# Kernel optimization log

Hardware: AMD Instinct MI355X
Metric: run time of the kernel (lower is better)

## Reference

```python
import jax, jax.numpy as jnp
import numpy as np
from jax import lax

MAP = 64  # spatial map resolution, hard-coded in the module


def setup_inputs() -> dict:
    key = jax.random.key(0)
    ks = jax.random.split(key, 6)
    B, N = 8, 17
    # valid boxes [x0,y0,x1,y1] inside the 64x64 map
    mins = jax.random.uniform(ks[0], (B, N, 2), jnp.float32) * 40.0
    sizes = jax.random.uniform(ks[1], (B, N, 2), jnp.float32) * 20.0 + 4.0
    bboxes = jnp.concatenate([mins, mins + sizes], axis=-1)  # [B,N,4]
    conv1_w = jax.random.normal(ks[2], (64, 2, 5, 5), jnp.float32) * 0.1
    conv1_b = jnp.zeros((64,), jnp.float32)
    conv2_w = jax.random.normal(ks[3], (32, 64, 5, 5), jnp.float32) * 0.05
    conv2_b = jnp.zeros((32,), jnp.float32)
    fc_w = jax.random.normal(ks[4], (512, 32), jnp.float32) * 0.1
    fc_b = jnp.zeros((512,), jnp.float32)
    return dict(bboxes=bboxes, conv1_w=conv1_w, conv1_b=conv1_b,
                conv2_w=conv2_w, conv2_b=conv2_b, fc_w=fc_w, fc_b=fc_b)


def _build_sp_maps(bboxes):
    # bboxes: [B,N,4] -> pairwise 2-channel binary maps [P, 2, 64, 64]
    B, N, _ = bboxes.shape
    iu, ju = jnp.triu_indices(N, k=1)           # P0 = N*(N-1)/2 pairs
    box_i = bboxes[:, iu]                       # [B,P0,4]
    box_j = bboxes[:, ju]                       # [B,P0,4]
    boxes = jnp.stack([box_i, box_j], axis=2)   # [B,P0,2,4]
    boxes = boxes.reshape(-1, 2, 4)             # [P,2,4]
    ys = jnp.arange(MAP, dtype=jnp.float32)[:, None]   # [64,1]
    xs = jnp.arange(MAP, dtype=jnp.float32)[None, :]   # [1,64]
    x0 = boxes[..., 0][..., None, None]
    y0 = boxes[..., 1][..., None, None]
    x1 = boxes[..., 2][..., None, None]
    y1 = boxes[..., 3][..., None, None]
    inside = (xs >= x0) & (xs < x1) & (ys >= y0) & (ys < y1)
    sp = inside.astype(bboxes.dtype)            # [P,2,64,64]
    # slicing tensor (batch, i, j) per pair
    P0 = iu.shape[0]
    b_idx = jnp.repeat(jnp.arange(B), P0)
    slicing = jnp.stack([b_idx, jnp.tile(iu, B), jnp.tile(ju, B)], axis=1)
    return sp, slicing


def _conv(x, w, b):
    y = lax.conv_general_dilated(x, w, (1, 1), 'VALID',
                                 dimension_numbers=('NCHW', 'OIHW', 'NCHW'))
    return y + b[None, :, None, None]


def _maxpool2(x):
    return lax.reduce_window(x, -jnp.inf, lax.max, (1, 1, 2, 2), (1, 1, 2, 2), 'VALID')


def reference(bboxes, conv1_w, conv1_b, conv2_w, conv2_b, fc_w, fc_b):
    sp, slicing = _build_sp_maps(bboxes)        # [P,2,64,64]
    h = _maxpool2(_conv(sp, conv1_w, conv1_b))  # [P,64,30,30]
    h = _maxpool2(_conv(h, conv2_w, conv2_b))   # [P,32,13,13]
    h = jnp.mean(h, axis=(2, 3))                # AvgPool(13) -> [P,32]
    feat = jax.nn.relu(h @ fc_w.T + fc_b)       # [P,512]
    return feat, slicing
```

## Files before the change

kernel.cpp:

```cpp
#include <hip/hip_runtime.h>
#include <hip/hip_bf16.h>


#define NPAIRS 1088
#define FEAT_SZ (NPAIRS * 512)

typedef float f32x16 __attribute__((ext_vector_type(16)));
typedef int v8i __attribute__((ext_vector_type(8)));
typedef float floatx2 __attribute__((ext_vector_type(2)));

#define WS_V 0
#define WS_C2B 14400
#define WS_BFRAG 14528

#define H1_PLANE 7200
#define H1_BYTES 57600
#define SM_V 57600
#define SM_HM 72000
#define SM_PART 72128
#define SMEM_BYTES 74176

__device__ __forceinline__ unsigned short f2bf(float f) {
  __hip_bfloat16 h = __float2bfloat16(f);
  unsigned short u;
  __builtin_memcpy(&u, &h, 2);
  return u;
}
__device__ __forceinline__ float bflo(unsigned int u) { return __uint_as_float(u << 16); }
__device__ __forceinline__ float bfhi(unsigned int u) { return __uint_as_float(u & 0xffff0000u); }

__device__ __forceinline__ void fp8x8_to_f32(uint2 u, float* f) {
  floatx2 t;
  t = __builtin_amdgcn_cvt_pk_f32_fp8((int)u.x, false); f[0] = t.x; f[1] = t.y;
  t = __builtin_amdgcn_cvt_pk_f32_fp8((int)u.x, true);  f[2] = t.x; f[3] = t.y;
  t = __builtin_amdgcn_cvt_pk_f32_fp8((int)u.y, false); f[4] = t.x; f[5] = t.y;
  t = __builtin_amdgcn_cvt_pk_f32_fp8((int)u.y, true);  f[6] = t.x; f[7] = t.y;
}

__device__ __forceinline__ void pair_ij(int k, int* pi, int* pj) {
  int i = 0, rem = k;
  while (rem >= 16 - i) { rem -= 16 - i; ++i; }
  *pi = i;
  *pj = i + 1 + rem;
}

__device__ __forceinline__ int stz(int z, int a, int b) {
  if (z >= a) {
    if (z >= b) return 0;
    if (z <= b - 5) return 5;
    return 5 + (b - z);
  }
  if (z >= a - 4) return a - z;
  return 0;
}

__global__ void prep_kernel(const float* __restrict__ w1, const float* __restrict__ b1,
                            const float* __restrict__ w2, float* __restrict__ out,
                            unsigned char* __restrict__ ws) {
  int tid = blockIdx.x * blockDim.x + threadIdx.x;

  if (tid < 12800) {
    int o = tid & 63;
    int q = tid >> 6;
    int sx = q % 10; q /= 10;
    int sy = q % 10;
    int c = q / 10;
    int ky0 = (sy <= 4) ? sy : 0;
    int ky1 = (sy == 0) ? 0 : ((sy <= 5) ? 5 : sy - 5);
    int kx0 = (sx <= 4) ? sx : 0;
    int kx1 = (sx == 0) ? 0 : ((sx <= 5) ? 5 : sx - 5);
    const float* w = w1 + (o * 2 + c) * 25;
    float v = 0.f;
    for (int ky = ky0; ky < ky1; ++ky)
      for (int kx = kx0; kx < kx1; ++kx) v += w[ky * 5 + kx];
    unsigned qv = __builtin_amdgcn_cvt_pk_fp8_f32(v, v, 0, false);
    ((unsigned char*)(ws + WS_V))[(c * 100 + sy * 10 + sx) * 72 + o] = (unsigned char)(qv & 0xFF);
  } else if (tid < 12832) {
    int oc = tid - 12800;
    float s = 0.f;
    for (int ic = 0; ic < 64; ++ic) {
      const float* wp = w2 + (oc * 64 + ic) * 25;
      float t = 0.f;
      for (int q2 = 0; q2 < 25; ++q2) t += wp[q2];
      s += b1[ic] * t;
    }
    ((float*)(ws + WS_C2B))[oc] = s;
  } else if (tid < 13920) {
    int p = tid - 12832;
    int b = p / 136, k = p % 136, i, j;
    pair_ij(k, &i, &j);
    out[FEAT_SZ + p * 3 + 0] = (float)b;
    out[FEAT_SZ + p * 3 + 1] = (float)i;
    out[FEAT_SZ + p * 3 + 2] = (float)j;
  } else if (tid < 26720) {
    int idx = tid - 13920;
    int d = idx & 7;
    int lane = (idx >> 3) & 63;
    int tap = idx >> 9;
    int n = lane & 31, h = lane >> 5;
    int icb = h * 32 + d * 4;
    float v0 = w2[(n * 64 + icb + 0) * 25 + tap];
    float v1 = w2[(n * 64 + icb + 1) * 25 + tap];
    float v2 = w2[(n * 64 + icb + 2) * 25 + tap];
    float v3 = w2[(n * 64 + icb + 3) * 25 + tap];
    unsigned q = 0;
    q = __builtin_amdgcn_cvt_pk_fp8_f32(v0, v1, q, false);
    q = __builtin_amdgcn_cvt_pk_fp8_f32(v2, v3, q, true);
    ((unsigned*)(ws + WS_BFRAG))[tap * 512 + lane * 8 + d] = q;
  }
}

__global__ __launch_bounds__(512, 4) void main_kernel(
    const float* __restrict__ bboxes, const float* __restrict__ b2,
    const float* __restrict__ fcw, const float* __restrict__ fcb,
    const unsigned char* __restrict__ ws, float* __restrict__ out) {
  __shared__ __align__(16) unsigned char smem[SMEM_BYTES];
  const int tid = threadIdx.x;
  const int lane = tid & 63;
  const int wid = tid >> 6;
  const int p = blockIdx.x;

  {
    const uint4* Vsrc = (const uint4*)(ws + WS_V);
    uint4* Vdst = (uint4*)(smem + SM_V);
    for (int i = tid; i < 900; i += 512) Vdst[i] = Vsrc[i];
  }

  int b = p / 136, k = p % 136, bi, bj;
  pair_ij(k, &bi, &bj);
  const float* bbA = bboxes + (b * 17 + bi) * 4;
  const float* bbB = bboxes + (b * 17 + bj) * 4;
  int ax[2], ay[2], bx[2], by[2];
  {
    auto cl = [](float v) { int t = (int)ceilf(v); return t < 0 ? 0 : (t > 64 ? 64 : t); };
    ax[0] = cl(bbA[0]); ay[0] = cl(bbA[1]); bx[0] = cl(bbA[2]); by[0] = cl(bbA[3]);
    ax[1] = cl(bbB[0]); ay[1] = cl(bbB[1]); bx[1] = cl(bbB[2]); by[1] = cl(bbB[3]);
  }

  int s0a = ay[0] - 4 < 0 ? 0 : ay[0] - 4;
  int s0b = ay[1] - 4 < 0 ? 0 : ay[1] - 4;
  int pre0 = s0a < s0b ? s0a : s0b;
  int e0a = by[0] < 60 ? by[0] : 60;
  int e0b = by[1] < 60 ? by[1] : 60;
  int pre1 = e0a > e0b ? e0a : e0b;
  int pr0 = pre0 >> 1, pr1 = (pre1 - 1) >> 1;
  int or0 = pr0 - 4 < 0 ? 0 : pr0 - 4;
  int or1 = pr1 > 25 ? 25 : pr1;
  int poslo = or0 * 26, poshi = (or1 + 1) * 26;
  int t_first = poslo >> 5;
  int t_last = (poshi - 1) >> 5;

  int pos_end = (t_last + 1) * 32; if (pos_end > 676) pos_end = 676;
  int zr0 = (t_first * 32) / 26;
  int zr1 = (pos_end - 1) / 26 + 4; if (zr1 > 29) zr1 = 29;

  __syncthreads();

  {
    for (int pos = tid; pos < 900; pos += 512) {
      int py = pos / 30, px = pos - py * 30;
      if (py < zr0 || py > zr1) continue;
      int oy = py * 2, ox = px * 2;
      int sy[2][2], sx[2][2];
#pragma unroll
      for (int c = 0; c < 2; ++c) {
        sy[c][0] = stz(oy, ay[c], by[c]);
        sy[c][1] = stz(oy + 1, ay[c], by[c]);
        sx[c][0] = stz(ox, ax[c], bx[c]);
        sx[c][1] = stz(ox + 1, ax[c], bx[c]);
      }
      bool e0 = ((sy[0][0] | sy[0][1]) == 0) || ((sx[0][0] | sx[0][1]) == 0);
      bool e1 = ((sy[1][0] | sy[1][1]) == 0) || ((sx[1][0] | sx[1][1]) == 0);
      unsigned hbase = (unsigned)pos * 8u;
      if (e0 && e1) {
#pragma unroll
        for (int g = 0; g < 8; ++g)
          *(uint2*)(smem + hbase + g * H1_PLANE) = make_uint2(0u, 0u);
        continue;
      }

      unsigned r0o[4], r1o[4];
#pragma unroll
      for (int dy = 0; dy < 2; ++dy)
#pragma unroll
        for (int dx = 0; dx < 2; ++dx) {
          r0o[dy * 2 + dx] = SM_V + (unsigned)(sy[0][dy] * 10 + sx[0][dx]) * 72u;
          r1o[dy * 2 + dx] = SM_V + 7200u + (unsigned)(sy[1][dy] * 10 + sx[1][dx]) * 72u;
        }

#pragma unroll
      for (int g = 0; g < 8; ++g) {
        float mx[8];
#pragma unroll
        for (int sp = 0; sp < 4; ++sp) {
          uint2 u0 = *(const uint2*)(smem + r0o[sp] + g * 8);
          uint2 u1 = *(const uint2*)(smem + r1o[sp] + g * 8);
          float a[8], c[8];
          fp8x8_to_f32(u0, a);
          fp8x8_to_f32(u1, c);
#pragma unroll
          for (int d = 0; d < 8; ++d) {
            float v = a[d] + c[d];
            mx[d] = (sp == 0) ? v : fmaxf(mx[d], v);
          }
        }
        unsigned q0 = 0, q1 = 0;
        q0 = __builtin_amdgcn_cvt_pk_fp8_f32(mx[0], mx[1], q0, false);
        q0 = __builtin_amdgcn_cvt_pk_fp8_f32(mx[2], mx[3], q0, true);
        q1 = __builtin_amdgcn_cvt_pk_fp8_f32(mx[4], mx[5], q1, false);
        q1 = __builtin_amdgcn_cvt_pk_fp8_f32(mx[6], mx[7], q1, true);
        *(uint2*)(smem + hbase + g * H1_PLANE) = make_uint2(q0, q1);
      }
    }
  }
  __syncthreads();

  const int oc = lane & 31;
  const float c2bb = ((const float*)(ws + WS_C2B))[oc] + b2[oc];

  int tb[3]; int acts[3]; unsigned vb[3]; bool anyact = false;
  const unsigned hvo = (unsigned)(lane >> 5) * (4u * H1_PLANE);
#pragma unroll
  for (int ti = 0; ti < 3; ++ti) {
    int t = t_first + wid + ti * 8;
    bool a = (t <= t_last);
    acts[ti] = __builtin_amdgcn_readfirstlane(a ? 1 : 0);
    anyact |= a;
    tb[ti] = t * 32;
    int pos = tb[ti] + (lane & 31);
    if (pos > 675) pos = 675;
    int oy2 = pos / 26, ox2 = pos - oy2 * 26;
    vb[ti] = (unsigned)(oy2 * 30 + ox2) * 8u + hvo;
  }

  f32x16 acc[3];
#pragma unroll
  for (int ti = 0; ti < 3; ++ti)
#pragma unroll
    for (int r = 0; r < 16; ++r) acc[ti][r] = 0.f;

  if (anyact) {
    const uint4* Bp = (const uint4*)(ws + WS_BFRAG);
    uint4 b0[3], b1[3];
#pragma unroll
    for (int t = 0; t < 3; ++t) {
      b0[t] = Bp[t * 128 + lane * 2 + 0];
      b1[t] = Bp[t * 128 + lane * 2 + 1];
    }
#pragma unroll
    for (int t = 0; t < 25; ++t) {
      const int sl = t % 3;
      uint4 bc0 = b0[sl], bc1 = b1[sl];
      if (t + 3 < 25) {
        b0[sl] = Bp[(t + 3) * 128 + lane * 2 + 0];
        b1[sl] = Bp[(t + 3) * 128 + lane * 2 + 1];
      }
      const int dtap = ((t / 5) * 30 + (t % 5)) * 8;
      v8i bop = (v8i){(int)bc0.x, (int)bc0.y, (int)bc0.z, (int)bc0.w,
                      (int)bc1.x, (int)bc1.y, (int)bc1.z, (int)bc1.w};
#pragma unroll
      for (int ti = 0; ti < 3; ++ti) {
        if (!acts[ti]) continue;
        uint2 a0 = *(const uint2*)(smem + vb[ti] + 0 * H1_PLANE + dtap);
        uint2 a1 = *(const uint2*)(smem + vb[ti] + 1 * H1_PLANE + dtap);
        uint2 a2 = *(const uint2*)(smem + vb[ti] + 2 * H1_PLANE + dtap);
        uint2 a3 = *(const uint2*)(smem + vb[ti] + 3 * H1_PLANE + dtap);
        v8i aop = (v8i){(int)a0.x, (int)a0.y, (int)a1.x, (int)a1.y,
                        (int)a2.x, (int)a2.y, (int)a3.x, (int)a3.y};
        acc[ti] = __builtin_amdgcn_mfma_scale_f32_32x32x64_f8f6f4(
            aop, bop, acc[ti], 0, 0, 0, 0x7F7F7F7F, 0, 0x7F7F7F7F);
      }
    }
  }
  __syncthreads();

  unsigned* c2w = (unsigned*)smem;
  const int oc353 = oc * 353;
#pragma unroll
  for (int ti = 0; ti < 3; ++ti) {
    if (!acts[ti]) continue;
#pragma unroll
    for (int rp = 0; rp < 8; ++rp) {
      int r = 2 * rp;
      int row = (r & 3) + 8 * (r >> 2) + 4 * (lane >> 5);
      int pos = tb[ti] + row;
      float lo = acc[ti][r] + c2bb, hi = acc[ti][r + 1] + c2bb;
      unsigned pk;
      asm("v_cvt_pk_bf16_f32 %0, %1, %2" : "=v"(pk) : "v"(lo), "v"(hi));
      c2w[oc353 + (pos >> 1)] = pk;
    }
  }
  {
    unsigned short cu = f2bf(c2bb);
    unsigned cupk = (unsigned)cu | ((unsigned)cu << 16);
#pragma unroll
    for (int ti = 0; ti < 3; ++ti) {
      int tf = wid + ti * 8;
      if (tf < 22 && (tf < t_first || tf > t_last)) {
#pragma unroll
        for (int rp = 0; rp < 8; ++rp) {
          int r = 2 * rp;
          int row = (r & 3) + 8 * (r >> 2) + 4 * (lane >> 5);
          int pos = tf * 32 + row;
          c2w[oc353 + (pos >> 1)] = cupk;
        }
      }
    }
  }
  __syncthreads();

  {
    float* partial = (float*)(smem + SM_PART);
    const unsigned* c2r = (const unsigned*)smem;
    int moc = lane & 31;
    int mi = wid * 2 + (lane >> 5);
    int m353 = moc * 353;
    float ssum = 0.f;
    for (int q = mi; q < 169; q += 16) {
      int py = q / 13, px = q - py * 13;
      int halfp = py * 26 + px;
      unsigned ua = c2r[m353 + halfp];
      unsigned ub = c2r[m353 + halfp + 13];
      float v00 = bflo(ua), v01 = bfhi(ua);
      float v10 = bflo(ub), v11 = bfhi(ub);
      ssum += fmaxf(fmaxf(v00, v01), fmaxf(v10, v11));
    }
    partial[mi * 32 + moc] = ssum;
  }
  __syncthreads();
  if (tid < 32) {
    const float* partial = (const float*)(smem + SM_PART);
    float s = 0.f;
#pragma unroll
    for (int mi = 0; mi < 16; ++mi) s += partial[mi * 32 + tid];
    ((float*)(smem + SM_HM))[tid] = s * (1.0f / 169.0f);
  }
  __syncthreads();

  {
    const float* hm = (const float*)(smem + SM_HM);
    const float4* wrow4 = (const float4*)(fcw + tid * 32);
    float a = fcb[tid];
#pragma unroll
    for (int q = 0; q < 8; ++q) {
      float4 w = wrow4[q];
      a = fmaf(hm[4 * q + 0], w.x, a);
      a = fmaf(hm[4 * q + 1], w.y, a);
      a = fmaf(hm[4 * q + 2], w.z, a);
      a = fmaf(hm[4 * q + 3], w.w, a);
    }
    out[p * 512 + tid] = fmaxf(a, 0.f);
  }
}

extern "C" void kernel_launch(void* const* d_in, const int* in_sizes, int n_in,
                              void* d_out, int out_size, void* d_ws, size_t ws_size,
                              hipStream_t stream) {
  const float* bboxes = (const float*)d_in[0];
  const float* w1 = (const float*)d_in[1];
  const float* b1 = (const float*)d_in[2];
  const float* w2 = (const float*)d_in[3];
  const float* b2 = (const float*)d_in[4];
  const float* fcw = (const float*)d_in[5];
  const float* fcb = (const float*)d_in[6];
  float* out = (float*)d_out;
  unsigned char* ws = (unsigned char*)d_ws;

  hipLaunchKernelGGL(prep_kernel, dim3(105), dim3(256), 0, stream, w1, b1, w2, out, ws);
  hipLaunchKernelGGL(main_kernel, dim3(NPAIRS), dim3(512), 0, stream, bboxes, b2, fcw, fcb, ws, out);
}
```

Before: 66.56 us.

## Repack conv1 output smem into 16-byte channel pairs and fast-path single-box pooling

Changes the layout of the pooled conv1 activation tile in shared memory. It goes from eight 8-byte channel-group planes to four 16-byte plane pairs, so stores and the MFMA A-operand loads use 128-bit accesses (two loads instead of four per tile). It also adds specialized paths for positions where only one box contributes or where all four pool taps map to the same precomputed value, which skips redundant conversions and max operations. The extra branches add divergence and code size, and they change the LDS bank access pattern.

```diff
diff --git a/kernel.cpp b/kernel.cpp
--- a/kernel.cpp
+++ b/kernel.cpp
@@ -13,7 +13,7 @@
 #define WS_C2B 14400
 #define WS_BFRAG 14528
 
-#define H1_PLANE 7200
+#define H1_PAIR 14400
 #define H1_BYTES 57600
 #define SM_V 57600
 #define SM_HM 72000
@@ -35,6 +35,13 @@
   t = __builtin_amdgcn_cvt_pk_f32_fp8((int)u.x, true);  f[2] = t.x; f[3] = t.y;
   t = __builtin_amdgcn_cvt_pk_f32_fp8((int)u.y, false); f[4] = t.x; f[5] = t.y;
   t = __builtin_amdgcn_cvt_pk_f32_fp8((int)u.y, true);  f[6] = t.x; f[7] = t.y;
+}
+
+__device__ __forceinline__ unsigned pack_fp8x4(float a, float b, float c, float d) {
+  unsigned q = 0;
+  q = __builtin_amdgcn_cvt_pk_fp8_f32(a, b, q, false);
+  q = __builtin_amdgcn_cvt_pk_fp8_f32(c, d, q, true);
+  return q;
 }
 
 __device__ __forceinline__ void pair_ij(int k, int* pi, int* pj) {
@@ -103,10 +110,7 @@
     float v1 = w2[(n * 64 + icb + 1) * 25 + tap];
     float v2 = w2[(n * 64 + icb + 2) * 25 + tap];
     float v3 = w2[(n * 64 + icb + 3) * 25 + tap];
-    unsigned q = 0;
-    q = __builtin_amdgcn_cvt_pk_fp8_f32(v0, v1, q, false);
-    q = __builtin_amdgcn_cvt_pk_fp8_f32(v2, v3, q, true);
-    ((unsigned*)(ws + WS_BFRAG))[tap * 512 + lane * 8 + d] = q;
+    ((unsigned*)(ws + WS_BFRAG))[tap * 512 + lane * 8 + d] = pack_fp8x4(v0, v1, v2, v3);
   }
 }
 
@@ -171,11 +175,55 @@
       }
       bool e0 = ((sy[0][0] | sy[0][1]) == 0) || ((sx[0][0] | sx[0][1]) == 0);
       bool e1 = ((sy[1][0] | sy[1][1]) == 0) || ((sx[1][0] | sx[1][1]) == 0);
-      unsigned hbase = (unsigned)pos * 8u;
+      unsigned hb = (unsigned)pos * 16u;
+
       if (e0 && e1) {
 #pragma unroll
-        for (int g = 0; g < 8; ++g)
-          *(uint2*)(smem + hbase + g * H1_PLANE) = make_uint2(0u, 0u);
+        for (int pp = 0; pp < 4; ++pp)
+          *(uint4*)(smem + pp * H1_PAIR + hb) = make_uint4(0u, 0u, 0u, 0u);
+        continue;
+      }
+
+      if (e0 || e1) {
+        int c = e0 ? 1 : 0;
+        unsigned ro[4];
+#pragma unroll
+        for (int dy = 0; dy < 2; ++dy)
+#pragma unroll
+          for (int dx = 0; dx < 2; ++dx)
+            ro[dy * 2 + dx] =
+                SM_V + (unsigned)c * 7200u + (unsigned)(sy[c][dy] * 10 + sx[c][dx]) * 72u;
+        bool same = (ro[1] == ro[0]) & (ro[2] == ro[0]) & (ro[3] == ro[0]);
+        if (same) {
+#pragma unroll
+          for (int pp = 0; pp < 4; ++pp) {
+            uint2 lo = *(const uint2*)(smem + ro[0] + pp * 16u);
+            uint2 hi = *(const uint2*)(smem + ro[0] + pp * 16u + 8u);
+            *(uint4*)(smem + pp * H1_PAIR + hb) = make_uint4(lo.x, lo.y, hi.x, hi.y);
+          }
+        } else {
+#pragma unroll
+          for (int pp = 0; pp < 4; ++pp) {
+            unsigned qv[4];
+#pragma unroll
+            for (int gg = 0; gg < 2; ++gg) {
+              int g = pp * 2 + gg;
+              float mx[8];
+#pragma unroll
+              for (int sp = 0; sp < 4; ++sp) {
+                uint2 u = *(const uint2*)(smem + ro[sp] + g * 8u);
+                float a[8];
+                fp8x8_to_f32(u, a);
+#pragma unroll
+                for (int d = 0; d < 8; ++d)
+                  mx[d] = (sp == 0) ? a[d] : fmaxf(mx[d], a[d]);
+              }
+              qv[2 * gg + 0] = pack_fp8x4(mx[0], mx[1], mx[2], mx[3]);
+              qv[2 * gg + 1] = pack_fp8x4(mx[4], mx[5], mx[6], mx[7]);
+            }
+            *(uint4*)(smem + pp * H1_PAIR + hb) = make_uint4(qv[0], qv[1], qv[2], qv[3]);
+          }
+        }
         continue;
       }
 
@@ -187,29 +235,51 @@
           r0o[dy * 2 + dx] = SM_V + (unsigned)(sy[0][dy] * 10 + sx[0][dx]) * 72u;
           r1o[dy * 2 + dx] = SM_V + 7200u + (unsigned)(sy[1][dy] * 10 + sx[1][dx]) * 72u;
         }
-
-#pragma unroll
-      for (int g = 0; g < 8; ++g) {
-        float mx[8];
-#pragma unroll
-        for (int sp = 0; sp < 4; ++sp) {
-          uint2 u0 = *(const uint2*)(smem + r0o[sp] + g * 8);
-          uint2 u1 = *(const uint2*)(smem + r1o[sp] + g * 8);
-          float a[8], c[8];
-          fp8x8_to_f32(u0, a);
-          fp8x8_to_f32(u1, c);
-#pragma unroll
-          for (int d = 0; d < 8; ++d) {
-            float v = a[d] + c[d];
-            mx[d] = (sp == 0) ? v : fmaxf(mx[d], v);
+      bool sameA = (r0o[1] == r0o[0]) & (r0o[2] == r0o[0]) & (r0o[3] == r0o[0]);
+      bool sameB = (r1o[1] == r1o[0]) & (r1o[2] == r1o[0]) & (r1o[3] == r1o[0]);
+      if (sameA && sameB) {
+#pragma unroll
+        for (int pp = 0; pp < 4; ++pp) {
+          unsigned qv[4];
+#pragma unroll
+          for (int gg = 0; gg < 2; ++gg) {
+            int g = pp * 2 + gg;
+            uint2 u0 = *(const uint2*)(smem + r0o[0] + g * 8u);
+            uint2 u1 = *(const uint2*)(smem + r1o[0] + g * 8u);
+            float a[8], c[8];
+            fp8x8_to_f32(u0, a);
+            fp8x8_to_f32(u1, c);
+            qv[2 * gg + 0] = pack_fp8x4(a[0] + c[0], a[1] + c[1], a[2] + c[2], a[3] + c[3]);
+            qv[2 * gg + 1] = pack_fp8x4(a[4] + c[4], a[5] + c[5], a[6] + c[6], a[7] + c[7]);
           }
+          *(uint4*)(smem + pp * H1_PAIR + hb) = make_uint4(qv[0], qv[1], qv[2], qv[3]);
         }
-        unsigned q0 = 0, q1 = 0;
-        q0 = __builtin_amdgcn_cvt_pk_fp8_f32(mx[0], mx[1], q0, false);
-        q0 = __builtin_amdgcn_cvt_pk_fp8_f32(mx[2], mx[3], q0, true);
-        q1 = __builtin_amdgcn_cvt_pk_fp8_f32(mx[4], mx[5], q1, false);
-        q1 = __builtin_amdgcn_cvt_pk_fp8_f32(mx[6], mx[7], q1, true);
-        *(uint2*)(smem + hbase + g * H1_PLANE) = make_uint2(q0, q1);
+      } else {
+#pragma unroll
+        for (int pp = 0; pp < 4; ++pp) {
+          unsigned qv[4];
+#pragma unroll
+          for (int gg = 0; gg < 2; ++gg) {
+            int g = pp * 2 + gg;
+            float mx[8];
+#pragma unroll
+            for (int sp = 0; sp < 4; ++sp) {
+              uint2 u0 = *(const uint2*)(smem + r0o[sp] + g * 8u);
+              uint2 u1 = *(const uint2*)(smem + r1o[sp] + g * 8u);
+              float a[8], c[8];
+              fp8x8_to_f32(u0, a);
+              fp8x8_to_f32(u1, c);
+#pragma unroll
+              for (int d = 0; d < 8; ++d) {
+                float v = a[d] + c[d];
+                mx[d] = (sp == 0) ? v : fmaxf(mx[d], v);
+              }
+            }
+            qv[2 * gg + 0] = pack_fp8x4(mx[0], mx[1], mx[2], mx[3]);
+            qv[2 * gg + 1] = pack_fp8x4(mx[4], mx[5], mx[6], mx[7]);
+          }
+          *(uint4*)(smem + pp * H1_PAIR + hb) = make_uint4(qv[0], qv[1], qv[2], qv[3]);
+        }
       }
     }
   }
@@ -219,7 +289,7 @@
   const float c2bb = ((const float*)(ws + WS_C2B))[oc] + b2[oc];
 
   int tb[3]; int acts[3]; unsigned vb[3]; bool anyact = false;
-  const unsigned hvo = (unsigned)(lane >> 5) * (4u * H1_PLANE);
+  const unsigned hvo16 = (unsigned)(lane >> 5) * (2u * H1_PAIR);
 #pragma unroll
   for (int ti = 0; ti < 3; ++ti) {
     int t = t_first + wid + ti * 8;
@@ -230,7 +300,7 @@
     int pos = tb[ti] + (lane & 31);
     if (pos > 675) pos = 675;
     int oy2 = pos / 26, ox2 = pos - oy2 * 26;
-    vb[ti] = (unsigned)(oy2 * 30 + ox2) * 8u + hvo;
+    vb[ti] = (unsigned)(oy2 * 30 + ox2) * 16u + hvo16;
   }
 
   f32x16 acc[3];
@@ -255,18 +325,16 @@
         b0[sl] = Bp[(t + 3) * 128 + lane * 2 + 0];
         b1[sl] = Bp[(t + 3) * 128 + lane * 2 + 1];
       }
-      const int dtap = ((t / 5) * 30 + (t % 5)) * 8;
+      const unsigned dtap16 = (unsigned)((t / 5) * 30 + (t % 5)) * 16u;
       v8i bop = (v8i){(int)bc0.x, (int)bc0.y, (int)bc0.z, (int)bc0.w,
                       (int)bc1.x, (int)bc1.y, (int)bc1.z, (int)bc1.w};
 #pragma unroll
       for (int ti = 0; ti < 3; ++ti) {
         if (!acts[ti]) continue;
-        uint2 a0 = *(const uint2*)(smem + vb[ti] + 0 * H1_PLANE + dtap);
-        uint2 a1 = *(const uint2*)(smem + vb[ti] + 1 * H1_PLANE + dtap);
-        uint2 a2 = *(const uint2*)(smem + vb[ti] + 2 * H1_PLANE + dtap);
-        uint2 a3 = *(const uint2*)(smem + vb[ti] + 3 * H1_PLANE + dtap);
-        v8i aop = (v8i){(int)a0.x, (int)a0.y, (int)a1.x, (int)a1.y,
-                        (int)a2.x, (int)a2.y, (int)a3.x, (int)a3.y};
+        uint4 r0 = *(const uint4*)(smem + vb[ti] + 0u * H1_PAIR + dtap16);
+        uint4 r1 = *(const uint4*)(smem + vb[ti] + 1u * H1_PAIR + dtap16);
+        v8i aop = (v8i){(int)r0.x, (int)r0.y, (int)r0.z, (int)r0.w,
+                        (int)r1.x, (int)r1.y, (int)r1.z, (int)r1.w};
         acc[ti] = __builtin_amdgcn_mfma_scale_f32_32x32x64_f8f6f4(
             aop, bop, acc[ti], 0, 0, 0, 0x7F7F7F7F, 0, 0x7F7F7F7F);
       }
```

Result: faster. 64.71 us (-2.8%).
